# Optimization experiments

Measured on AMD Instinct MI355X. Metric: run time of the kernel, lower is better.

The kernel has to match this reference:

```python
import jax, jax.numpy as jnp
import numpy as np

NUM_KERNELS = 8
KERNEL_SIZES = [2 ** i for i in range(1, NUM_KERNELS + 1)]


def setup_inputs() -> dict:
    key = jax.random.key(0)
    x = jax.random.uniform(key, (32, 1, 1024, 1024), dtype=jnp.float32)
    return {"x": x}


def _plogp(p):
    # p * log2(p), safely 0 at p == 0 (log2(1) == 0)
    ps = jnp.where(p > 0, p, 1.0)
    return ps * jnp.log2(ps)


def reference(x):
    # Slice_windows(num_kernels=8, mode='entropy', to_binary=False)
    B, C, H, W = x.shape
    cols = []
    for k in KERNEL_SIZES:
        if k > H or k > W:
            cols.append(jnp.zeros((B,), dtype=x.dtype))
            continue
        Hk, Wk = H // k, W // k
        n = k * k * C
        # non-overlapping window sums == sum-pooling with stride k
        xs = x[:, :, : Hk * k, : Wk * k].reshape(B, C, Hk, k, Wk, k)
        s = xs.sum(axis=(1, 3, 5))            # (B, Hk, Wk)
        p1 = s / n
        p0 = 1.0 - p1
        entropy = -_plogp(p0) - _plogp(p1)    # Shannon entropy per window
        cols.append(entropy.mean(axis=(1, 2)))  # average over all windows
    return jnp.stack(cols, axis=1)  # (B, num_kernels)
```

## Files before the change

### kernel.cpp

```cpp
#include <hip/hip_runtime.h>

#define IMG 1024

__device__ __forceinline__ float ent(float s, float inv_n) {
    float p1 = s * inv_n;
    float p0 = 1.0f - p1;
    float l1 = (p1 > 0.0f) ? __log2f(p1) : 0.0f;
    float l0 = (p0 > 0.0f) ? __log2f(p0) : 0.0f;
    return -(p0 * l0 + p1 * l1);
}

__device__ __forceinline__ float bfly_sum(float v) {
#pragma unroll
    for (int m = 32; m >= 1; m >>= 1) v += __shfl_xor(v, m);
    return v;
}

__global__ __launch_bounds__(256, 4) void slice_k1(const float* __restrict__ x,
                                                   float* __restrict__ ws) {
    const int b    = blockIdx.x >> 6;
    const int tile = blockIdx.x & 63;
    const int tr = tile >> 3, tc = tile & 7;
    const int t = threadIdx.x;
    const int w = t >> 6, lane = t & 63;
    const int hi = lane >> 5, lo = lane & 31;

    const float* p = x + (size_t)b * (IMG * IMG)
                       + (size_t)(tr * 128 + w * 32 + hi) * IMG + (tc * 128 + lo * 4);

    float4 v[16];
#pragma unroll
    for (int i = 0; i < 16; ++i)
        v[i] = *(const float4*)(p + (size_t)(2 * i) * IMG);

    float e2 = 0.f, e4 = 0.f, e8 = 0.f, e16 = 0.f;
    float s4p[16];
#pragma unroll
    for (int i = 0; i < 16; ++i) {
        float h0 = v[i].x + v[i].y;
        float h1 = v[i].z + v[i].w;
        float s2a = h0 + __shfl_xor(h0, 32);
        float s2b = h1 + __shfl_xor(h1, 32);
        e2 += ent(s2a, 0.25f) + ent(s2b, 0.25f);
        s4p[i] = s2a + s2b;
    }
    float s4[8], s8[4], s16[2];
#pragma unroll
    for (int j = 0; j < 8; ++j) {
        s4[j] = s4p[2 * j] + s4p[2 * j + 1];
        e4 += ent(s4[j], 1.f / 16.f);
    }
#pragma unroll
    for (int m = 0; m < 4; ++m) {
        float t8 = s4[2 * m] + s4[2 * m + 1];
        s8[m] = t8 + __shfl_xor(t8, 1);
        e8 += ent(s8[m], 1.f / 64.f);
    }
#pragma unroll
    for (int q = 0; q < 2; ++q) {
        float t16 = s8[2 * q] + s8[2 * q + 1];
        s16[q] = t16 + __shfl_xor(t16, 2);
        e16 += ent(s16[q], 1.f / 256.f);
    }
    float t32 = s16[0] + s16[1];
    float s32 = t32 + __shfl_xor(t32, 4);
    float e32 = ent(s32, 1.f / 1024.f);

    float E2  = bfly_sum(e2);
    float E4  = bfly_sum(e4);
    float E8  = bfly_sum(e8);
    float E16 = bfly_sum(e16);
    float E32 = bfly_sum(e32);

    __shared__ float wl[4][5];
    __shared__ float wl32[4][4];
    if (lane == 0) {
        wl[w][0] = E2 * 0.5f;   wl[w][1] = E4 * 0.5f;  wl[w][2] = E8 * 0.25f;
        wl[w][3] = E16 * 0.125f; wl[w][4] = E32 * 0.0625f;
    }
    if (hi == 0 && (lo & 7) == 0) wl32[w][lo >> 3] = s32;
    __syncthreads();

    if (t < 8) {
        float r;
        if (t < 5) {
            r = wl[0][t] + wl[1][t] + wl[2][t] + wl[3][t];
        } else {
            float s64a = wl32[0][0] + wl32[0][1] + wl32[1][0] + wl32[1][1];
            float s64b = wl32[0][2] + wl32[0][3] + wl32[1][2] + wl32[1][3];
            float s64c = wl32[2][0] + wl32[2][1] + wl32[3][0] + wl32[3][1];
            float s64d = wl32[2][2] + wl32[2][3] + wl32[3][2] + wl32[3][3];
            if (t == 5) {
                r = ent(s64a, 1.f / 4096.f) + ent(s64b, 1.f / 4096.f)
                  + ent(s64c, 1.f / 4096.f) + ent(s64d, 1.f / 4096.f);
            } else {
                float s128 = s64a + s64b + s64c + s64d;
                r = (t == 6) ? ent(s128, 1.f / 16384.f) : s128;
            }
        }
        ws[(size_t)blockIdx.x * 8 + t] = r;
    }
}

__global__ __launch_bounds__(64) void slice_k2(const float* __restrict__ ws,
                                               float* __restrict__ out) {
    const int b = blockIdx.x, l = threadIdx.x;
    const float4* g = (const float4*)(ws + ((size_t)b * 64 + l) * 8);
    float4 u0 = g[0], u1 = g[1];
    float v[8] = {u0.x, u0.y, u0.z, u0.w, u1.x, u1.y, u1.z, u1.w};

    float s256 = v[7] + __shfl_xor(v[7], 1); s256 += __shfl_xor(s256, 8);
    float e256 = ent(s256, 1.f / 65536.f);
    float E256 = e256 + __shfl_xor(e256, 2); E256 += __shfl_xor(E256, 4);
    E256 += __shfl_xor(E256, 16);  E256 += __shfl_xor(E256, 32);

    float sums[7];
#pragma unroll
    for (int j = 0; j < 7; ++j) sums[j] = bfly_sum(v[j]);

    if (l == 0) {
        const float invw[7] = {1.f / 262144.f, 1.f / 65536.f, 1.f / 16384.f,
                               1.f / 4096.f,   1.f / 1024.f,  1.f / 256.f, 1.f / 64.f};
        float* o = out + b * 8;
#pragma unroll
        for (int j = 0; j < 7; ++j) o[j] = sums[j] * invw[j];
        o[7] = E256 * (1.f / 16.f);
    }
}

extern "C" void kernel_launch(void* const* d_in, const int* in_sizes, int n_in,
                              void* d_out, int out_size, void* d_ws, size_t ws_size,
                              hipStream_t stream) {
    const float* x = (const float*)d_in[0];
    float* out = (float*)d_out;
    float* ws  = (float*)d_ws;

    slice_k1<<<32 * 64, 256, 0, stream>>>(x, ws);
    slice_k2<<<32, 64, 0, stream>>>(ws, out);
}
```

Baseline: 190.3 us.

## Retile blocks to 64x256 strips with contiguous row loads and in-thread 2x2 sums

Each block now covers a 64x256 tile, and each thread reads 16 consecutive rows, so each wave reads full 1KB row segments. The 2x2 and 4x4 window sums are formed inside a thread instead of with cross-lane shuffles. The 32/64 levels are reduced in shared memory, and the 128/256 levels move to the second kernel, which reads the per-block 64-window sums. This removes shuffles and the old two-rows-per-wave access pattern, at the cost of a more complex cross-kernel reduction layout.

```diff
diff --git a/kernel.cpp b/kernel.cpp
--- a/kernel.cpp
+++ b/kernel.cpp
@@ -18,113 +18,115 @@
 
 __global__ __launch_bounds__(256, 4) void slice_k1(const float* __restrict__ x,
                                                    float* __restrict__ ws) {
-    const int b    = blockIdx.x >> 6;
-    const int tile = blockIdx.x & 63;
-    const int tr = tile >> 3, tc = tile & 7;
+    const int b   = blockIdx.x >> 6;
+    const int tau = blockIdx.x & 63;
+    const int ty = tau >> 2, tx = tau & 3;
     const int t = threadIdx.x;
-    const int w = t >> 6, lane = t & 63;
-    const int hi = lane >> 5, lo = lane & 31;
+    const int w = t >> 6, l = t & 63;
 
     const float* p = x + (size_t)b * (IMG * IMG)
-                       + (size_t)(tr * 128 + w * 32 + hi) * IMG + (tc * 128 + lo * 4);
-
+                       + (size_t)(ty * 64 + w * 16) * IMG + (tx * 256 + l * 4);
     float4 v[16];
 #pragma unroll
     for (int i = 0; i < 16; ++i)
-        v[i] = *(const float4*)(p + (size_t)(2 * i) * IMG);
+        v[i] = *(const float4*)(p + (size_t)i * IMG);
 
-    float e2 = 0.f, e4 = 0.f, e8 = 0.f, e16 = 0.f;
-    float s4p[16];
+    float e2 = 0.f, e4 = 0.f, e8 = 0.f;
+    float s4h[8], s4[4];
 #pragma unroll
-    for (int i = 0; i < 16; ++i) {
-        float h0 = v[i].x + v[i].y;
-        float h1 = v[i].z + v[i].w;
-        float s2a = h0 + __shfl_xor(h0, 32);
-        float s2b = h1 + __shfl_xor(h1, 32);
+    for (int i = 0; i < 8; ++i) {
+        float4 a = v[2 * i], c = v[2 * i + 1];
+        float s2a = a.x + a.y + c.x + c.y;
+        float s2b = a.z + a.w + c.z + c.w;
         e2 += ent(s2a, 0.25f) + ent(s2b, 0.25f);
-        s4p[i] = s2a + s2b;
+        s4h[i] = s2a + s2b;
     }
-    float s4[8], s8[4], s16[2];
 #pragma unroll
-    for (int j = 0; j < 8; ++j) {
-        s4[j] = s4p[2 * j] + s4p[2 * j + 1];
+    for (int j = 0; j < 4; ++j) {
+        s4[j] = s4h[2 * j] + s4h[2 * j + 1];
         e4 += ent(s4[j], 1.f / 16.f);
     }
+    float s8[2];
 #pragma unroll
-    for (int m = 0; m < 4; ++m) {
+    for (int m = 0; m < 2; ++m) {
         float t8 = s4[2 * m] + s4[2 * m + 1];
         s8[m] = t8 + __shfl_xor(t8, 1);
         e8 += ent(s8[m], 1.f / 64.f);
     }
-#pragma unroll
-    for (int q = 0; q < 2; ++q) {
-        float t16 = s8[2 * q] + s8[2 * q + 1];
-        s16[q] = t16 + __shfl_xor(t16, 2);
-        e16 += ent(s16[q], 1.f / 256.f);
-    }
-    float t32 = s16[0] + s16[1];
-    float s32 = t32 + __shfl_xor(t32, 4);
-    float e32 = ent(s32, 1.f / 1024.f);
+    float t16 = s8[0] + s8[1];
+    float s16 = t16 + __shfl_xor(t16, 2);
+    float e16 = ent(s16, 1.f / 256.f);
 
-    float E2  = bfly_sum(e2);
-    float E4  = bfly_sum(e4);
-    float E8  = bfly_sum(e8);
-    float E16 = bfly_sum(e16);
-    float E32 = bfly_sum(e32);
+    float E2 = bfly_sum(e2), E4 = bfly_sum(e4);
+    float E8 = bfly_sum(e8), E16 = bfly_sum(e16);
 
-    __shared__ float wl[4][5];
-    __shared__ float wl32[4][4];
-    if (lane == 0) {
-        wl[w][0] = E2 * 0.5f;   wl[w][1] = E4 * 0.5f;  wl[w][2] = E8 * 0.25f;
-        wl[w][3] = E16 * 0.125f; wl[w][4] = E32 * 0.0625f;
-    }
-    if (hi == 0 && (lo & 7) == 0) wl32[w][lo >> 3] = s32;
+    __shared__ float s16l[4][16];
+    __shared__ float wle[4][4];
+    if ((l & 3) == 0) s16l[w][l >> 2] = s16;
+    if (l == 0) { wle[w][0] = E2; wle[w][1] = E4; wle[w][2] = E8; wle[w][3] = E16; }
     __syncthreads();
 
-    if (t < 8) {
-        float r;
-        if (t < 5) {
-            r = wl[0][t] + wl[1][t] + wl[2][t] + wl[3][t];
-        } else {
-            float s64a = wl32[0][0] + wl32[0][1] + wl32[1][0] + wl32[1][1];
-            float s64b = wl32[0][2] + wl32[0][3] + wl32[1][2] + wl32[1][3];
-            float s64c = wl32[2][0] + wl32[2][1] + wl32[3][0] + wl32[3][1];
-            float s64d = wl32[2][2] + wl32[2][3] + wl32[3][2] + wl32[3][3];
-            if (t == 5) {
-                r = ent(s64a, 1.f / 4096.f) + ent(s64b, 1.f / 4096.f)
-                  + ent(s64c, 1.f / 4096.f) + ent(s64d, 1.f / 4096.f);
-            } else {
-                float s128 = s64a + s64b + s64c + s64d;
-                r = (t == 6) ? ent(s128, 1.f / 16384.f) : s128;
-            }
+    if (t < 16) {
+        int r = t >> 3, c = t & 7;
+        float s32 = s16l[2 * r][2 * c] + s16l[2 * r][2 * c + 1]
+                  + s16l[2 * r + 1][2 * c] + s16l[2 * r + 1][2 * c + 1];
+        float e32 = ent(s32, 1.f / 1024.f);
+        float a = s32 + __shfl_xor(s32, 1);
+        float s64v = a + __shfl_xor(a, 8);
+        float e64 = ent(s64v, 1.f / 4096.f);
+#pragma unroll
+        for (int m = 8; m >= 1; m >>= 1) {
+            e32 += __shfl_xor(e32, m);
+            e64 += __shfl_xor(e64, m);
         }
-        ws[(size_t)blockIdx.x * 8 + t] = r;
+        if (t < 8 && (t & 1) == 0)
+            ws[b * 256 + ty * 16 + tx * 4 + (t >> 1)] = s64v;
+        if (t == 0) {
+            float* rec = ws + 8192 + (size_t)blockIdx.x * 8;
+            rec[0] = wle[0][0] + wle[1][0] + wle[2][0] + wle[3][0];
+            rec[1] = wle[0][1] + wle[1][1] + wle[2][1] + wle[3][1];
+            rec[2] = (wle[0][2] + wle[1][2] + wle[2][2] + wle[3][2]) * 0.5f;
+            rec[3] = (wle[0][3] + wle[1][3] + wle[2][3] + wle[3][3]) * 0.25f;
+            rec[4] = e32;
+            rec[5] = e64 * 0.25f;
+            rec[6] = 0.f; rec[7] = 0.f;
+        }
     }
 }
 
 __global__ __launch_bounds__(64) void slice_k2(const float* __restrict__ ws,
                                                float* __restrict__ out) {
     const int b = blockIdx.x, l = threadIdx.x;
-    const float4* g = (const float4*)(ws + ((size_t)b * 64 + l) * 8);
-    float4 u0 = g[0], u1 = g[1];
-    float v[8] = {u0.x, u0.y, u0.z, u0.w, u1.x, u1.y, u1.z, u1.w};
+    const float* rec = ws + 8192 + ((size_t)b * 64 + l) * 8;
+    float4 u0 = *(const float4*)rec;
+    float u4 = rec[4], u5 = rec[5];
+    float T0 = bfly_sum(u0.x), T1 = bfly_sum(u0.y);
+    float T2 = bfly_sum(u0.z), T3 = bfly_sum(u0.w);
+    float T4 = bfly_sum(u4),   T5 = bfly_sum(u5);
 
-    float s256 = v[7] + __shfl_xor(v[7], 1); s256 += __shfl_xor(s256, 8);
+    float4 s = *(const float4*)(ws + (size_t)b * 256 + l * 4);
+    float4 sv;
+    sv.x = s.x + __shfl_xor(s.x, 4);
+    sv.y = s.y + __shfl_xor(s.y, 4);
+    sv.z = s.z + __shfl_xor(s.z, 4);
+    sv.w = s.w + __shfl_xor(s.w, 4);
+    float a128 = sv.x + sv.y, b128 = sv.z + sv.w;
+    float e128 = ent(a128, 1.f / 16384.f) + ent(b128, 1.f / 16384.f);
+    float h = a128 + b128;
+    float s256 = h + __shfl_xor(h, 8);
     float e256 = ent(s256, 1.f / 65536.f);
-    float E256 = e256 + __shfl_xor(e256, 2); E256 += __shfl_xor(E256, 4);
-    E256 += __shfl_xor(E256, 16);  E256 += __shfl_xor(E256, 32);
-
-    float sums[7];
-#pragma unroll
-    for (int j = 0; j < 7; ++j) sums[j] = bfly_sum(v[j]);
+    float T6 = bfly_sum(e128), T7 = bfly_sum(e256);
 
     if (l == 0) {
-        const float invw[7] = {1.f / 262144.f, 1.f / 65536.f, 1.f / 16384.f,
-                               1.f / 4096.f,   1.f / 1024.f,  1.f / 256.f, 1.f / 64.f};
         float* o = out + b * 8;
-#pragma unroll
-        for (int j = 0; j < 7; ++j) o[j] = sums[j] * invw[j];
-        o[7] = E256 * (1.f / 16.f);
+        o[0] = T0 * (1.f / 262144.f);
+        o[1] = T1 * (1.f / 65536.f);
+        o[2] = T2 * (1.f / 16384.f);
+        o[3] = T3 * (1.f / 4096.f);
+        o[4] = T4 * (1.f / 1024.f);
+        o[5] = T5 * (1.f / 256.f);
+        o[6] = T6 * 0.5f * (1.f / 64.f);
+        o[7] = T7 * 0.25f * (1.f / 16.f);
     }
 }
 
```

Measured after the change: 186.8 us. Within noise of the previous version (-1.9%).
